# Performance work log

Hardware: AMD Instinct MI355X
Metric: run time of the kernel (lower is better)

## Reference

```python
import jax, jax.numpy as jnp
import numpy as np

NEG = -1e30  # finite stand-in for -inf so logaddexp grads stay clean
ADVERSARY_WEIGHT = 0.5


def _bfctc(logits, targets, act_lens, tgt_lens):
    """Blank-free CTC negative log-likelihood, size_average=True (mean over batch).

    logits: (T, B, C) unnormalized activations (log_softmax applied internally,
            as in warp-ctc style bindings).
    targets: (B, U) int label ids (padding beyond tgt_lens is ignored).
    Alignment lattice: at each frame stay on the same label or advance one
    label (no blank state):
        alpha[t, u] = logaddexp(alpha[t-1, u], alpha[t-1, u-1]) + logp[t, y_u]
    Loss per utterance = -alpha[act_len-1, tgt_len-1].
    """
    T, B, C = logits.shape
    U = targets.shape[1]
    logprobs = jax.nn.log_softmax(logits, axis=-1)  # (T,B,C)
    idx = jnp.broadcast_to(targets[None], (T, B, U))
    lp = jnp.take_along_axis(logprobs, idx, axis=2)  # (T,B,U) logp of each target label per frame

    alpha0 = lp[0] + jnp.where(jnp.arange(U) == 0, 0.0, NEG)[None, :]  # (B,U)

    def step(alpha, inp):
        lp_t, t = inp
        shifted = jnp.concatenate(
            [jnp.full((B, 1), NEG, alpha.dtype), alpha[:, :-1]], axis=1)
        new = jnp.logaddexp(alpha, shifted) + lp_t
        # freeze alpha once past this utterance's frame length
        alpha = jnp.where((t < act_lens)[:, None], new, alpha)
        return alpha, None

    alpha, _ = jax.lax.scan(step, alpha0, (lp[1:], jnp.arange(1, T)))
    loss_b = -jnp.take_along_axis(alpha, (tgt_lens - 1)[:, None], axis=1)[:, 0]
    return jnp.mean(loss_b)  # size_average=True


def reference(x, W, b, ctc_target_p1, ctc_target_p2, ctc_acts_lens,
              ctc_target_lens_p1, ctc_target_lens_p2):
    # output_layer projection then (B,T,C) -> (T,B,C), float32 cast
    logits = (x @ W + b)
    acts = jnp.transpose(logits, (1, 0, 2)).astype(jnp.float32)
    l1 = _bfctc(acts, ctc_target_p1, ctc_acts_lens, ctc_target_lens_p1)
    l2 = _bfctc(acts, ctc_target_p2, ctc_acts_lens, ctc_target_lens_p2)
    return (l1 - ADVERSARY_WEIGHT * l2, l1, l2)


def setup_inputs() -> dict:
    B, T, U, D, C = 16, 2000, 400, 512, 4096
    key = jax.random.key(0)
    k = jax.random.split(key, 8)
    x = jax.random.normal(k[0], (B, T, D), dtype=jnp.float32)
    W = jax.random.normal(k[1], (D, C), dtype=jnp.float32) * 0.02
    b = jnp.zeros((C,), dtype=jnp.float32)
    tgt1 = jax.random.randint(k[2], (B, U), 0, C)
    tgt2 = jax.random.randint(k[3], (B, U), 0, C)
    # frame lengths in [T//2, T) so every target (U<=400) has a valid alignment
    act_lens = jax.random.randint(k[4], (B,), T // 2, T)
    tlen1 = jax.random.randint(k[5], (B,), 1, U + 1)
    tlen2 = jax.random.randint(k[6], (B,), 1, U + 1)
    return {
        "x": x, "W": W, "b": b,
        "ctc_target_p1": tgt1, "ctc_target_p2": tgt2,
        "ctc_acts_lens": act_lens,
        "ctc_target_lens_p1": tlen1, "ctc_target_lens_p2": tlen2,
    }
```

## Files before the change

### kernel.cpp

```cpp
#include <hip/hip_runtime.h>
#include <hip/hip_bf16.h>
#include <stdint.h>

constexpr int B_ = 16;
constexpr int T_ = 2000;
constexpr int U_ = 400;
constexpr int D_ = 512;
constexpr int C_ = 4096;
constexpr int U2P_ = 1024;
constexpr float LN2F = 0.6931471805599453f;

typedef __attribute__((ext_vector_type(8))) short bf16x8;
typedef __attribute__((ext_vector_type(4))) float f32x4;
typedef __attribute__((ext_vector_type(8))) unsigned short us8;

__device__ __forceinline__ ushort f2bf(float f) {
  uint32_t u = __builtin_bit_cast(uint32_t, f);
  uint32_t r = (u + 0x7fffu + ((u >> 16) & 1u)) >> 16;
  return (ushort)r;
}

__device__ __forceinline__ float bf2f(ushort h) {
  return __builtin_bit_cast(float, (uint32_t)h << 16);
}

__device__ __forceinline__ void async_copy16(const void* gptr, void* ldsptr) {
  __builtin_amdgcn_global_load_lds(
      (const __attribute__((address_space(1))) uint32_t*)gptr,
      (__attribute__((address_space(3))) uint32_t*)ldsptr,
      16, 0, 0);
}

__global__ void cvt_bf16_k(const float* __restrict__ in, ushort* __restrict__ out, int n4) {
  int i = blockIdx.x * blockDim.x + threadIdx.x;
  int stride = gridDim.x * blockDim.x;
  for (; i < n4; i += stride) {
    float4 v = ((const float4*)in)[i];
    ushort4 o;
    o.x = f2bf(v.x); o.y = f2bf(v.y); o.z = f2bf(v.z); o.w = f2bf(v.w);
    ((ushort4*)out)[i] = o;
  }
}

__global__ void transposeW_k(const float* __restrict__ W, ushort* __restrict__ Wt) {
  __shared__ float tile[32][33];
  int c0 = blockIdx.x * 32, d0 = blockIdx.y * 32;
  int tx = threadIdx.x, ty = threadIdx.y;
  #pragma unroll
  for (int i = 0; i < 4; ++i) {
    int r = ty + i * 8;
    tile[r][tx] = W[(size_t)(d0 + r) * C_ + c0 + tx];
  }
  __syncthreads();
  #pragma unroll
  for (int i = 0; i < 4; ++i) {
    int r = ty + i * 8;
    Wt[(size_t)(c0 + r) * D_ + d0 + tx] = f2bf(tile[tx][r]);
  }
}

__global__ void gatherW_k(const ushort* __restrict__ Wt, const float* __restrict__ bias,
                          const int* __restrict__ t1, const int* __restrict__ t2,
                          ushort* __restrict__ Wgt, float* __restrict__ biasg) {
  int u2 = blockIdx.x;
  int b = blockIdx.y;
  int tid = threadIdx.x;
  int set = u2 >= 512;
  int us = u2 - (set ? 512 : 0);
  int c = (us < U_) ? (set ? t2 : t1)[b * U_ + us] : -1;
  ushort4 v; v.x = 0; v.y = 0; v.z = 0; v.w = 0;
  if (c >= 0) v = *(const ushort4*)(Wt + (size_t)c * D_ + tid * 4);
  *(ushort4*)(Wgt + ((size_t)b * U2P_ + u2) * D_ + tid * 4) = v;
  if (tid == 0) biasg[b * U2P_ + u2] = (c >= 0) ? bias[c] : 0.f;
}

template <bool IS_LP>
__global__ __launch_bounds__(512, 2) void gemm8_k(
    const ushort* __restrict__ A, const ushort* __restrict__ Bt,
    const float* __restrict__ biasp, float* __restrict__ lsesum,
    ushort* __restrict__ cbuf) {
  constexpr int K = D_;
  constexpr int NKT = K / 32;
  __shared__ __align__(16) ushort As[4][8192];
  __shared__ __align__(16) ushort Bs[4][8192];
  const int tid = threadIdx.x;
  const int wid = tid >> 6, lane = tid & 63;
  const int wr = wid >> 2, wc = wid & 3;
  const int h = lane >> 4, lr = lane & 15;
  const int bn = blockIdx.x, bm = blockIdx.y, bz = blockIdx.z;

  const ushort* Ab = A + ((size_t)(IS_LP ? bz * T_ : 0) + (size_t)bm * 256) * K;
  const ushort* Bb = Bt + ((size_t)(IS_LP ? bz * U2P_ : 0) + (size_t)bn * 256) * K;

  auto stageA = [&](int buf, int kt, int j) {
    int o = (j * 8 + wid) * 64 + lane;
    int row = o >> 2;
    int g = ((o & 3) - (row >> 1)) & 3;
    async_copy16(Ab + (size_t)row * K + kt * 32 + g * 8,
                 &As[buf][(size_t)(j * 8 + wid) * 512]);
  };
  auto stageB = [&](int buf, int kt, int j) {
    int o = (j * 8 + wid) * 64 + lane;
    int row = o >> 2;
    int g = ((o & 3) - (row >> 1)) & 3;
    async_copy16(Bb + (size_t)row * K + kt * 32 + g * 8,
                 &Bs[buf][(size_t)(j * 8 + wid) * 512]);
  };

  f32x4 acc[8][4];
  #pragma unroll
  for (int mi = 0; mi < 8; ++mi)
    #pragma unroll
    for (int ni = 0; ni < 4; ++ni) {
      f32x4 z = {0.f, 0.f, 0.f, 0.f};
      acc[mi][ni] = z;
    }

  for (int kt = 0; kt < 3; ++kt) {
    stageA(kt, kt, 0); stageA(kt, kt, 1);
    stageB(kt, kt, 0); stageB(kt, kt, 1);
  }

  for (int kt = 0; kt < NKT; ++kt) {
    const int buf = kt & 3;
    if (kt <= NKT - 3)      asm volatile("s_waitcnt vmcnt(8)" ::: "memory");
    else if (kt == NKT - 2) asm volatile("s_waitcnt vmcnt(4)" ::: "memory");
    else                    asm volatile("s_waitcnt vmcnt(0)" ::: "memory");
    __builtin_amdgcn_s_barrier();
    __builtin_amdgcn_sched_barrier(0);

    bf16x8 bfr[4];
    #pragma unroll
    for (int ni = 0; ni < 4; ++ni) {
      int row = wc * 64 + ni * 16 + lr;
      int c16 = (h + (row >> 1)) & 3;
      bfr[ni] = *(const bf16x8*)(&Bs[buf][row * 32 + c16 * 8]);
    }
    {
      bf16x8 af[4];
      #pragma unroll
      for (int mi = 0; mi < 4; ++mi) {
        int row = wr * 128 + mi * 16 + lr;
        int c16 = (h + (row >> 1)) & 3;
        af[mi] = *(const bf16x8*)(&As[buf][row * 32 + c16 * 8]);
      }
      if (kt + 3 < NKT) {
        stageA((kt + 3) & 3, kt + 3, 0);
        stageA((kt + 3) & 3, kt + 3, 1);
      }
      __builtin_amdgcn_s_barrier();
      __builtin_amdgcn_s_setprio(1);
      #pragma unroll
      for (int mi = 0; mi < 4; ++mi)
        #pragma unroll
        for (int ni = 0; ni < 4; ++ni)
          acc[mi][ni] = __builtin_amdgcn_mfma_f32_16x16x32_bf16(af[mi], bfr[ni], acc[mi][ni], 0, 0, 0);
      __builtin_amdgcn_s_setprio(0);
      __builtin_amdgcn_s_barrier();
    }
    {
      bf16x8 af[4];
      #pragma unroll
      for (int mi = 0; mi < 4; ++mi) {
        int row = wr * 128 + (mi + 4) * 16 + lr;
        int c16 = (h + (row >> 1)) & 3;
        af[mi] = *(const bf16x8*)(&As[buf][row * 32 + c16 * 8]);
      }
      if (kt + 3 < NKT) {
        stageB((kt + 3) & 3, kt + 3, 0);
        stageB((kt + 3) & 3, kt + 3, 1);
      }
      __builtin_amdgcn_s_barrier();
      __builtin_amdgcn_s_setprio(1);
      #pragma unroll
      for (int mi = 0; mi < 4; ++mi)
        #pragma unroll
        for (int ni = 0; ni < 4; ++ni)
          acc[mi + 4][ni] = __builtin_amdgcn_mfma_f32_16x16x32_bf16(af[mi], bfr[ni], acc[mi + 4][ni], 0, 0, 0);
      __builtin_amdgcn_s_setprio(0);
    }
  }

  if constexpr (!IS_LP) {
    float bv[4];
    #pragma unroll
    for (int ni = 0; ni < 4; ++ni)
      bv[ni] = biasp[bn * 256 + wc * 64 + ni * 16 + lr];
    #pragma unroll
    for (int mi = 0; mi < 8; ++mi) {
      #pragma unroll
      for (int r = 0; r < 4; ++r) {
        float s = 0.f;
        #pragma unroll
        for (int ni = 0; ni < 4; ++ni) s += __expf(acc[mi][ni][r] + bv[ni]);
        s += __shfl_xor(s, 1);
        s += __shfl_xor(s, 2);
        s += __shfl_xor(s, 4);
        s += __shfl_xor(s, 8);
        if (lr == 0) {
          int grow = bm * 256 + wr * 128 + mi * 16 + h * 4 + r;
          atomicAdd(&lsesum[grow], s);
        }
      }
    }
  } else {
    float bv[4];
    #pragma unroll
    for (int ni = 0; ni < 4; ++ni)
      bv[ni] = biasp[bz * U2P_ + bn * 256 + wc * 64 + ni * 16 + lr];
    #pragma unroll
    for (int mi = 0; mi < 8; ++mi) {
      #pragma unroll
      for (int r = 0; r < 4; ++r) {
        int t = bm * 256 + wr * 128 + mi * 16 + h * 4 + r;
        if (t < T_) {
          #pragma unroll
          for (int ni = 0; ni < 4; ++ni) {
            int u2 = bn * 256 + wc * 64 + ni * 16 + lr;
            int set = u2 >> 9;
            int us = u2 & 511;
            float val = (us < U_) ? __expf(acc[mi][ni][r] + bv[ni]) : 0.f;
            cbuf[((size_t)(bz * 2 + set) * T_ + t) * 512 + us] = f2bf(val);
          }
        }
      }
    }
  }
}

__global__ void lse_reduce_k(const float* __restrict__ lsesum, const int* __restrict__ act_lens,
                             float* __restrict__ S) {
  int b = blockIdx.x;
  int al = act_lens[b];
  float s = 0.f;
  for (int t = threadIdx.x; t < al; t += blockDim.x)
    s += logf(lsesum[b * T_ + t]);
  #pragma unroll
  for (int off = 32; off >= 1; off >>= 1) s += __shfl_xor(s, off);
  __shared__ float wsum[4];
  int w = threadIdx.x >> 6, lane = threadIdx.x & 63;
  if (lane == 0) wsum[w] = s;
  __syncthreads();
  if (threadIdx.x == 0) S[b] = wsum[0] + wsum[1] + wsum[2] + wsum[3];
}

__global__ __launch_bounds__(64) void bfctc_scan_k(
    const ushort* __restrict__ cbuf, const int* __restrict__ act_lens,
    const int* __restrict__ tl1, const int* __restrict__ tl2,
    float* __restrict__ rawloss) {
  int bi = blockIdx.x;
  int b = bi >> 1, set = bi & 1;
  int lane = threadIdx.x;
  int al = act_lens[b];
  int tl = (set ? tl2 : tl1)[b];
  const char* base = (const char*)cbuf + (size_t)bi * T_ * 1024 + lane * 16;

  float alpha[8];
  int E = 0;
  float bscale;

  {
    us8 c0 = *(const us8*)(base);
    float iv0 = bf2f(c0[0]);
    #pragma unroll
    for (int r = 0; r < 8; ++r) alpha[r] = 0.f;
    if (lane == 0) alpha[0] = iv0;
    bscale = (lane >= 50) ? 0.f : 1.0f;
  }

  auto step1 = [&](us8 c8) {
    int pi = __builtin_amdgcn_update_dpp(
        0, __builtin_bit_cast(int, alpha[7]), 0x138 , 0xf, 0xf, true);
    float prev = __builtin_bit_cast(float, pi) * bscale;
    float c[8];
    #pragma unroll
    for (int r = 0; r < 8; ++r) c[r] = bf2f(c8[r]);
    #pragma unroll
    for (int r = 7; r >= 1; --r)
      alpha[r] = (alpha[r] + alpha[r - 1]) * c[r];
    alpha[0] = (alpha[0] + prev) * c[0];
  };

  auto rescale = [&]() {
    float m01 = fmaxf(alpha[0], alpha[1]);
    float m23 = fmaxf(alpha[2], alpha[3]);
    float m45 = fmaxf(alpha[4], alpha[5]);
    float m67 = fmaxf(alpha[6], alpha[7]);
    float m = fmaxf(fmaxf(m01, m23), fmaxf(m45, m67));
    int mb = __builtin_bit_cast(int, m);
    bool dead = (mb == 0);
    int ei = ((mb >> 23) & 255) - 127;
    float s = __builtin_bit_cast(float, (127 - ei) << 23);
    #pragma unroll
    for (int r = 0; r < 8; ++r) alpha[r] *= s;
    if (!dead) E += ei;
    int pe = __builtin_amdgcn_update_dpp(0, E, 0x138, 0xf, 0xf, true);
    if (dead) E = pe;
    int dE = pe - E;
    dE = dE < -126 ? -126 : (dE > 126 ? 126 : dE);
    bscale = __builtin_bit_cast(float, (127 + dE) << 23);
    if (lane >= 50) bscale = 0.f;
  };

  us8 B0[8], B1[8], B2[8], B3[8];
  auto load0 = [&](int blk) {
    const char* p = base + (size_t)(1 + 8 * blk) * 1024;
    #pragma unroll
    for (int i = 0; i < 8; ++i) B0[i] = *(const us8*)(p + i * 1024);
  };
  auto load1 = [&](int blk) {
    const char* p = base + (size_t)(1 + 8 * blk) * 1024;
    #pragma unroll
    for (int i = 0; i < 8; ++i) B1[i] = *(const us8*)(p + i * 1024);
  };
  auto load2 = [&](int blk) {
    const char* p = base + (size_t)(1 + 8 * blk) * 1024;
    #pragma unroll
    for (int i = 0; i < 8; ++i) B2[i] = *(const us8*)(p + i * 1024);
  };
  auto load3 = [&](int blk) {
    const char* p = base + (size_t)(1 + 8 * blk) * 1024;
    #pragma unroll
    for (int i = 0; i < 8; ++i) B3[i] = *(const us8*)(p + i * 1024);
  };
  auto comp0 = [&]() {
    #pragma unroll
    for (int i = 0; i < 8; ++i) step1(B0[i]);
  };
  auto comp1 = [&]() {
    #pragma unroll
    for (int i = 0; i < 8; ++i) step1(B1[i]);
  };
  auto comp2 = [&]() {
    #pragma unroll
    for (int i = 0; i < 8; ++i) step1(B2[i]);
  };
  auto comp3 = [&]() {
    #pragma unroll
    for (int i = 0; i < 8; ++i) step1(B3[i]);
  };

  int S = al - 1;
  int nb = S >> 3;
  load0(0); load1(1); load2(2); load3(3);
  int j = 0;
  while (j + 4 <= nb) {
    comp0(); rescale(); load0(j + 4);
    comp1(); rescale(); load1(j + 5);
    comp2(); rescale(); load2(j + 6);
    comp3(); rescale(); load3(j + 7);
    j += 4;
  }
  if (j < nb)     { comp0(); rescale(); }
  if (j + 1 < nb) { comp1(); rescale(); }
  if (j + 2 < nb) { comp2(); rescale(); }
  for (int t = 1 + 8 * nb; t <= S; ++t) {
    us8 c = *(const us8*)(base + (size_t)t * 1024);
    step1(c);
  }

  int ui = tl - 1, lt = ui >> 3, rt = ui & 7;
  float v = alpha[0];
  #pragma unroll
  for (int r = 1; r < 8; ++r) v = (rt == r) ? alpha[r] : v;
  float tot = (__builtin_amdgcn_logf(v) + (float)E) * LN2F;
  tot = __shfl(tot, lt);
  if (lane == 0) rawloss[bi] = tot;
}

__global__ void combine_k(const float* __restrict__ S, const float* __restrict__ raw,
                          float* __restrict__ out) {
  int lane = threadIdx.x;
  float d1 = 0.f, d2 = 0.f;
  if (lane < 16) {
    d1 = S[lane] - raw[lane * 2 + 0];
    d2 = S[lane] - raw[lane * 2 + 1];
  }
  #pragma unroll
  for (int off = 8; off >= 1; off >>= 1) {
    d1 += __shfl_xor(d1, off);
    d2 += __shfl_xor(d2, off);
  }
  if (lane == 0) {
    float l1 = d1 * (1.f / 16.f), l2 = d2 * (1.f / 16.f);
    out[0] = l1 - 0.5f * l2;
    out[1] = l1;
    out[2] = l2;
  }
}

extern "C" void kernel_launch(void* const* d_in, const int* in_sizes, int n_in,
                              void* d_out, int out_size, void* d_ws, size_t ws_size,
                              hipStream_t stream) {
  const float* x    = (const float*)d_in[0];
  const float* W    = (const float*)d_in[1];
  const float* bias = (const float*)d_in[2];
  const int* t1  = (const int*)d_in[3];
  const int* t2  = (const int*)d_in[4];
  const int* al  = (const int*)d_in[5];
  const int* tl1 = (const int*)d_in[6];
  const int* tl2 = (const int*)d_in[7];
  float* out = (float*)d_out;

  char* ws = (char*)d_ws;
  size_t off = 0;
  auto alloc = [&](size_t bytes) -> char* {
    char* p = ws + off;
    off += (bytes + 255) & ~(size_t)255;
    return p;
  };
  ushort* xb     = (ushort*)alloc((size_t)B_ * T_ * D_ * 2);
  ushort* Wt     = (ushort*)alloc((size_t)C_ * D_ * 2);
  ushort* Wgt    = (ushort*)alloc((size_t)B_ * U2P_ * D_ * 2);
  float*  biasg  = (float*)alloc((size_t)B_ * U2P_ * 4);
  float*  lsesum = (float*)alloc((size_t)B_ * T_ * 4);
  ushort* cbuf   = (ushort*)alloc((size_t)2 * B_ * T_ * 512 * 2);
  alloc(65536);
  float*  Sb     = (float*)alloc(B_ * 4);
  float*  rawl   = (float*)alloc(2 * B_ * 4);
  (void)ws_size; (void)in_sizes; (void)n_in; (void)out_size;

  (void)hipMemsetAsync(lsesum, 0, (size_t)B_ * T_ * 4, stream);

  cvt_bf16_k<<<2048, 256, 0, stream>>>(x, xb, B_ * T_ * D_ / 4);
  transposeW_k<<<dim3(C_ / 32, D_ / 32), dim3(32, 8), 0, stream>>>(W, Wt);
  gatherW_k<<<dim3(U2P_, B_), 128, 0, stream>>>(Wt, bias, t1, t2, Wgt, biasg);

  gemm8_k<false><<<dim3(C_ / 256, (B_ * T_) / 256, 1), 512, 0, stream>>>(
      xb, Wt, bias, lsesum, nullptr);
  gemm8_k<true><<<dim3(U2P_ / 256, 2048 / 256, B_), 512, 0, stream>>>(
      xb, Wgt, biasg, nullptr, cbuf);

  lse_reduce_k<<<B_, 256, 0, stream>>>(lsesum, al, Sb);
  bfctc_scan_k<<<2 * B_, 64, 0, stream>>>(cbuf, al, tl1, tl2, rawl);
  combine_k<<<1, 64, 0, stream>>>(Sb, rawl, out);
}
```

Before: 478.5 us.

## Restructure GEMM main loop into double-buffered 64-wide K steps

```diff
diff --git a/kernel.cpp b/kernel.cpp
--- a/kernel.cpp
+++ b/kernel.cpp
@@ -80,9 +80,8 @@
     const float* __restrict__ biasp, float* __restrict__ lsesum,
     ushort* __restrict__ cbuf) {
   constexpr int K = D_;
-  constexpr int NKT = K / 32;
-  __shared__ __align__(16) ushort As[4][8192];
-  __shared__ __align__(16) ushort Bs[4][8192];
+  __shared__ __align__(16) ushort As[2][2][8192];
+  __shared__ __align__(16) ushort Bs[2][2][8192];
   const int tid = threadIdx.x;
   const int wid = tid >> 6, lane = tid & 63;
   const int wr = wid >> 2, wc = wid & 3;
@@ -92,19 +91,19 @@
   const ushort* Ab = A + ((size_t)(IS_LP ? bz * T_ : 0) + (size_t)bm * 256) * K;
   const ushort* Bb = Bt + ((size_t)(IS_LP ? bz * U2P_ : 0) + (size_t)bn * 256) * K;
 
-  auto stageA = [&](int buf, int kt, int j) {
-    int o = (j * 8 + wid) * 64 + lane;
-    int row = o >> 2;
-    int g = ((o & 3) - (row >> 1)) & 3;
-    async_copy16(Ab + (size_t)row * K + kt * 32 + g * 8,
-                 &As[buf][(size_t)(j * 8 + wid) * 512]);
-  };
-  auto stageB = [&](int buf, int kt, int j) {
-    int o = (j * 8 + wid) * 64 + lane;
-    int row = o >> 2;
-    int g = ((o & 3) - (row >> 1)) & 3;
-    async_copy16(Bb + (size_t)row * K + kt * 32 + g * 8,
-                 &Bs[buf][(size_t)(j * 8 + wid) * 512]);
+  auto frag = [&](const ushort* chunk, int row) -> bf16x8 {
+    int c16 = (h + (row >> 1)) & 3;
+    return *(const bf16x8*)(chunk + row * 32 + c16 * 8);
+  };
+  auto stage = [&](ushort* chunk, const ushort* gsrc) {
+    #pragma unroll
+    for (int j = 0; j < 2; ++j) {
+      int o = j * 512 + tid;
+      int row = o >> 2;
+      int g = ((o & 3) - (row >> 1)) & 3;
+      async_copy16(gsrc + (size_t)row * K + g * 8,
+                   chunk + (j * 512 + wid * 64) * 8);
+    }
   };
 
   f32x4 acc[8][4];
@@ -116,69 +115,80 @@
       acc[mi][ni] = z;
     }
 
-  for (int kt = 0; kt < 3; ++kt) {
-    stageA(kt, kt, 0); stageA(kt, kt, 1);
-    stageB(kt, kt, 0); stageB(kt, kt, 1);
-  }
-
-  for (int kt = 0; kt < NKT; ++kt) {
-    const int buf = kt & 3;
-    if (kt <= NKT - 3)      asm volatile("s_waitcnt vmcnt(8)" ::: "memory");
-    else if (kt == NKT - 2) asm volatile("s_waitcnt vmcnt(4)" ::: "memory");
-    else                    asm volatile("s_waitcnt vmcnt(0)" ::: "memory");
+  stage(&As[0][0][0], Ab);
+  stage(&Bs[0][0][0], Bb);
+  stage(&As[0][1][0], Ab + 32);
+  stage(&Bs[0][1][0], Bb + 32);
+
+  #pragma unroll 2
+  for (int kt = 0; kt < 8; ++kt) {
+    const int c = kt & 1, nx = c ^ 1;
+    const ushort* A0 = &As[c][0][0];
+    const ushort* A1 = &As[c][1][0];
+    const ushort* B0 = &Bs[c][0][0];
+    const ushort* B1 = &Bs[c][1][0];
+    const ushort* Asrc = Ab + (kt + 1) * 64;
+    const ushort* Bsrc = Bb + (kt + 1) * 64;
+    bf16x8 bf0[4], bf1[4], af[4];
+
+    asm volatile("s_waitcnt vmcnt(4)" ::: "memory");
     __builtin_amdgcn_s_barrier();
     __builtin_amdgcn_sched_barrier(0);
-
-    bf16x8 bfr[4];
-    #pragma unroll
-    for (int ni = 0; ni < 4; ++ni) {
-      int row = wc * 64 + ni * 16 + lr;
-      int c16 = (h + (row >> 1)) & 3;
-      bfr[ni] = *(const bf16x8*)(&Bs[buf][row * 32 + c16 * 8]);
-    }
-    {
-      bf16x8 af[4];
-      #pragma unroll
-      for (int mi = 0; mi < 4; ++mi) {
-        int row = wr * 128 + mi * 16 + lr;
-        int c16 = (h + (row >> 1)) & 3;
-        af[mi] = *(const bf16x8*)(&As[buf][row * 32 + c16 * 8]);
-      }
-      if (kt + 3 < NKT) {
-        stageA((kt + 3) & 3, kt + 3, 0);
-        stageA((kt + 3) & 3, kt + 3, 1);
-      }
-      __builtin_amdgcn_s_barrier();
-      __builtin_amdgcn_s_setprio(1);
-      #pragma unroll
-      for (int mi = 0; mi < 4; ++mi)
-        #pragma unroll
-        for (int ni = 0; ni < 4; ++ni)
-          acc[mi][ni] = __builtin_amdgcn_mfma_f32_16x16x32_bf16(af[mi], bfr[ni], acc[mi][ni], 0, 0, 0);
-      __builtin_amdgcn_s_setprio(0);
-      __builtin_amdgcn_s_barrier();
-    }
-    {
-      bf16x8 af[4];
-      #pragma unroll
-      for (int mi = 0; mi < 4; ++mi) {
-        int row = wr * 128 + (mi + 4) * 16 + lr;
-        int c16 = (h + (row >> 1)) & 3;
-        af[mi] = *(const bf16x8*)(&As[buf][row * 32 + c16 * 8]);
-      }
-      if (kt + 3 < NKT) {
-        stageB((kt + 3) & 3, kt + 3, 0);
-        stageB((kt + 3) & 3, kt + 3, 1);
-      }
-      __builtin_amdgcn_s_barrier();
-      __builtin_amdgcn_s_setprio(1);
-      #pragma unroll
-      for (int mi = 0; mi < 4; ++mi)
-        #pragma unroll
-        for (int ni = 0; ni < 4; ++ni)
-          acc[mi + 4][ni] = __builtin_amdgcn_mfma_f32_16x16x32_bf16(af[mi], bfr[ni], acc[mi + 4][ni], 0, 0, 0);
-      __builtin_amdgcn_s_setprio(0);
-    }
+    #pragma unroll
+    for (int ni = 0; ni < 4; ++ni) bf0[ni] = frag(B0, wc * 64 + ni * 16 + lr);
+    #pragma unroll
+    for (int mi = 0; mi < 4; ++mi) af[mi] = frag(A0, wr * 128 + mi * 16 + lr);
+    if (kt < 7) stage(&As[nx][0][0], Asrc);
+    __builtin_amdgcn_s_setprio(1);
+    #pragma unroll
+    for (int mi = 0; mi < 4; ++mi)
+      #pragma unroll
+      for (int ni = 0; ni < 4; ++ni)
+        acc[mi][ni] = __builtin_amdgcn_mfma_f32_16x16x32_bf16(af[mi], bf0[ni], acc[mi][ni], 0, 0, 0);
+    __builtin_amdgcn_s_setprio(0);
+
+    __builtin_amdgcn_s_barrier();
+    __builtin_amdgcn_sched_barrier(0);
+    #pragma unroll
+    for (int mi = 0; mi < 4; ++mi) af[mi] = frag(A0, wr * 128 + (mi + 4) * 16 + lr);
+    if (kt < 7) stage(&Bs[nx][0][0], Bsrc);
+    __builtin_amdgcn_s_setprio(1);
+    #pragma unroll
+    for (int mi = 0; mi < 4; ++mi)
+      #pragma unroll
+      for (int ni = 0; ni < 4; ++ni)
+        acc[mi + 4][ni] = __builtin_amdgcn_mfma_f32_16x16x32_bf16(af[mi], bf0[ni], acc[mi + 4][ni], 0, 0, 0);
+    __builtin_amdgcn_s_setprio(0);
+
+    if (kt < 7) { asm volatile("s_waitcnt vmcnt(4)" ::: "memory"); }
+    else        { asm volatile("s_waitcnt vmcnt(0)" ::: "memory"); }
+    __builtin_amdgcn_s_barrier();
+    __builtin_amdgcn_sched_barrier(0);
+    #pragma unroll
+    for (int ni = 0; ni < 4; ++ni) bf1[ni] = frag(B1, wc * 64 + ni * 16 + lr);
+    #pragma unroll
+    for (int mi = 0; mi < 4; ++mi) af[mi] = frag(A1, wr * 128 + mi * 16 + lr);
+    if (kt < 7) stage(&As[nx][1][0], Asrc + 32);
+    __builtin_amdgcn_s_setprio(1);
+    #pragma unroll
+    for (int mi = 0; mi < 4; ++mi)
+      #pragma unroll
+      for (int ni = 0; ni < 4; ++ni)
+        acc[mi][ni] = __builtin_amdgcn_mfma_f32_16x16x32_bf16(af[mi], bf1[ni], acc[mi][ni], 0, 0, 0);
+    __builtin_amdgcn_s_setprio(0);
+
+    __builtin_amdgcn_s_barrier();
+    __builtin_amdgcn_sched_barrier(0);
+    #pragma unroll
+    for (int mi = 0; mi < 4; ++mi) af[mi] = frag(A1, wr * 128 + (mi + 4) * 16 + lr);
+    if (kt < 7) stage(&Bs[nx][1][0], Bsrc + 32);
+    __builtin_amdgcn_s_setprio(1);
+    #pragma unroll
+    for (int mi = 0; mi < 4; ++mi)
+      #pragma unroll
+      for (int ni = 0; ni < 4; ++ni)
+        acc[mi + 4][ni] = __builtin_amdgcn_mfma_f32_16x16x32_bf16(af[mi], bf1[ni], acc[mi + 4][ni], 0, 0, 0);
+    __builtin_amdgcn_s_setprio(0);
   }
 
   if constexpr (!IS_LP) {
```

New measurement: 470.4 us. No clear change (-1.7%).
